# Optimization experiments

Hardware: AMD Instinct MI355X
Metric: run time of the kernel (lower is better)

## Reference

```python
import jax, jax.numpy as jnp
import numpy as np

D = 128        # feature dim (hard-coded 128 split in source)
C = 16         # number of classes
N_S = 1600     # support set size (C * 100 shots)
Q = 32768      # number of query samples
HID = 128      # Class_Adap hidden width


def _class_centers(support_feat_inv, support_features, support_labels):
    # per-class mean of both support tensors (ComputeClassCenters)
    ones = jnp.ones((support_labels.shape[0],), support_feat_inv.dtype)
    counts = jax.ops.segment_sum(ones, support_labels, num_segments=C)
    counts = jnp.maximum(counts, 1.0)[:, None]                     # [C,1]
    mean_s = jax.ops.segment_sum(support_feat_inv, support_labels, num_segments=C) / counts   # [C,D]
    pre_s = jax.ops.segment_sum(support_features, support_labels, num_segments=C) / counts    # [C,D]
    return mean_s, pre_s


def setup_inputs() -> dict:
    key = jax.random.key(0)
    ks = jax.random.split(key, 6)
    return {
        "support_feat_inv": jax.random.normal(ks[0], (N_S, D), jnp.float32),
        "support_features": jax.random.normal(ks[1], (N_S, D), jnp.float32),
        "query_features": jax.random.normal(ks[2], (Q, D), jnp.float32),
        "W1": jax.random.normal(ks[3], (2 * D + 1, HID), jnp.float32) * 0.05,
        "b1": jnp.zeros((HID,), jnp.float32),
        "W2": jax.random.normal(ks[4], (HID, 1), jnp.float32) * 0.05,
        "b2": jnp.zeros((1,), jnp.float32),
        "support_labels": jax.random.randint(ks[5], (N_S,), 0, C),
        "query_labels": jax.random.randint(jax.random.fold_in(key, 7), (Q,), 0, C),
    }


def reference(support_feat_inv, support_features, query_features, W1, b1, W2, b2,
              support_labels, query_labels) -> jnp.ndarray:
    mean_s, pre_s = _class_centers(support_feat_inv, support_features, support_labels)
    q = query_features[:, None, :]                                  # [Q,1,D]
    gated = jax.nn.sigmoid(mean_s)[None, :, :] * q                  # [Q,C,D]
    q_full = jnp.broadcast_to(q, gated.shape)                       # [Q,C,D]
    inp = jnp.concatenate([q_full, gated], axis=-1)                 # [Q,C,2D]
    # AdaptiveAvgPool2d((None, D)) on [C,1,2D]: average adjacent pairs along last dim
    pooled = inp.reshape(Q, C, D, 2).mean(axis=-1)                  # [Q,C,D]
    # inner/outer product: sum(pre_support * query) per class
    outer = jnp.sum(pre_s[None, :, :] * q, axis=-1, keepdims=True)  # [Q,C,1]
    ext = jnp.concatenate([inp, outer], axis=-1)                    # [Q,C,2D+1]
    # Class_Adap tiny MLP -> per-class scalar weight
    h = jax.nn.relu(jnp.einsum('qce,eh->qch', ext, W1) + b1)        # [Q,C,HID]
    w = jax.nn.sigmoid(jnp.einsum('qch,ho->qco', h, W2) + b2)       # [Q,C,1]
    agg = jnp.sum(pooled * w, axis=1)                               # [Q,D]
    return agg + query_features                                     # residual (query_feature[0])
```

## Files before the change

kernel.cpp:

```cpp
#include <hip/hip_runtime.h>
#include <hip/hip_bf16.h>
#include <stdint.h>

#define DD 128
#define CC 16
#define NS 1600
#define QQ 32768
#define NBLK 64
#define PLW 65

typedef __attribute__((ext_vector_type(8))) short short8;
typedef __attribute__((ext_vector_type(4))) short short4v;
typedef __attribute__((ext_vector_type(4))) float f32x4;

__device__ inline short f2bf(float x) {
  union { float f; uint32_t u; } v; v.f = x;
  uint32_t r = (v.u + 0x7FFFu + ((v.u >> 16) & 1u)) >> 16;
  return (short)r;
}

__device__ inline uint32_t pk2bf(float lo, float hi) {
  __hip_bfloat162 h = __float22bfloat162_rn(make_float2(lo, hi));
  union { __hip_bfloat162 h2; uint32_t u; } v; v.h2 = h;
  return v.u;
}

__device__ inline float bfbits2f(uint32_t hi16bits) {
  union { uint32_t u; float f; } v; v.u = hi16bits;
  return v.f;
}

__global__ __launch_bounds__(256) void prep_kernel(
    const float* __restrict__ sfi, const float* __restrict__ sf,
    const int* __restrict__ labels, const float* __restrict__ qf,
    float* __restrict__ partA, float* __restrict__ partB,
    float* __restrict__ pcnt, short* __restrict__ qbf) {
  const int t = threadIdx.x;

  if (blockIdx.x >= NBLK) {
    const size_t cb = (size_t)(blockIdx.x - NBLK) * (128 * DD);
#pragma unroll
    for (int i = 0; i < 16; ++i) {
      const size_t off = cb + ((size_t)i * 256 + t) * 4;
      f32x4 f = *(const f32x4*)(qf + off);
      union { short4v s; uint32_t u[2]; } r;
      r.u[0] = pk2bf(f[0], f[1]);
      r.u[1] = pk2bf(f[2], f[3]);
      *(short4v*)(qbf + off) = r.s;
    }
    return;
  }

  __shared__ float accA[2][CC][DD];
  __shared__ float accB[2][CC][DD];
  __shared__ float cnt[2][CC];
  const int d = t & 127, s = t >> 7;
  for (int i = t; i < 2 * CC * DD; i += 256) {
    ((float*)accA)[i] = 0.f;
    ((float*)accB)[i] = 0.f;
  }
  if (t < 2 * CC) ((float*)cnt)[t] = 0.f;
  __syncthreads();

  const int base = blockIdx.x * (NS / NBLK);
  for (int i = s; i < NS / NBLK; i += 2) {
    const int r = base + i;
    const int lbl = labels[r];
    accA[s][lbl][d] += sfi[(size_t)r * DD + d];
    accB[s][lbl][d] += sf[(size_t)r * DD + d];
    if (d == 0) cnt[s][lbl] += 1.f;
  }
  __syncthreads();

  float* pa = partA + (size_t)blockIdx.x * (CC * DD);
  float* pb = partB + (size_t)blockIdx.x * (CC * DD);
  for (int i = t; i < CC * DD; i += 256) {
    pa[i] = ((float*)accA)[i] + ((float*)accA)[CC * DD + i];
    pb[i] = ((float*)accB)[i] + ((float*)accB)[CC * DD + i];
  }
  if (t < CC) pcnt[blockIdx.x * CC + t] = cnt[0][t] + cnt[1][t];
}

__global__ __launch_bounds__(256) void build_wt_kernel(
    const float* __restrict__ W1, const float* __restrict__ partA,
    const float* __restrict__ partB, const float* __restrict__ pcnt,
    float* __restrict__ sg_out, short* __restrict__ WtTg) {
  __shared__ float sgc[DD], prc[DD];
  const int c = blockIdx.x, t = threadIdx.x;

  float cnt = 0.f;
  for (int b = 0; b < NBLK; ++b) cnt += pcnt[b * CC + c];
  cnt = fmaxf(cnt, 1.f);
  if (t < 128) {
    float a = 0.f;
    for (int b = 0; b < NBLK; ++b) a += partA[(size_t)b * (CC * DD) + c * DD + t];
    const float m = a / cnt;
    const float s = 1.f / (1.f + expf(-m));
    sgc[t] = s;
    sg_out[c * DD + t] = s;
  } else {
    const int d = t - 128;
    float a = 0.f;
    for (int b = 0; b < NBLK; ++b) a += partB[(size_t)b * (CC * DD) + c * DD + d];
    prc[d] = a / cnt;
  }
  __syncthreads();

  for (int it = 0; it < 8; ++it) {
    const int u = it * 256 + t;
    const int w_ = u >> 8;
    const int kb = (u >> 6) & 3;
    const int lane = u & 63;
    const int j = w_ * 16 + (lane & 15);
    const int e0 = kb * 32 + (lane >> 4) * 8;
    short8 r;
#pragma unroll
    for (int rr = 0; rr < 8; ++rr) {
      const int e = e0 + rr;
      float v = W1[e * DD + j] + sgc[e] * W1[(DD + e) * DD + j] +
                prc[e] * W1[2 * DD * DD + j];
      r[rr] = f2bf(v);
    }
    *(short8*)(WtTg + ((size_t)c * 2048 + u) * 8) = r;
  }
}

__global__ __launch_bounds__(512, 4) void main_kernel(
    const short* __restrict__ qbf, const short* __restrict__ WtTg,
    const float* __restrict__ b1, const float* __restrict__ W2,
    const float* __restrict__ b2, const float* __restrict__ sg,
    float* __restrict__ out) {
  __shared__ float p_pln[4 * 64 * PLW];
  __shared__ float w_lds[64][17];

  const int tid = threadIdx.x;
  const int lane = tid & 63;
  const int w = tid >> 6;
  const int l15 = lane & 15, l4 = lane >> 4;
  const int qbase = blockIdx.x * 64;

  short8 bq[4][4];
#pragma unroll
  for (int qn = 0; qn < 4; ++qn) {
    const short* qrow = qbf + (size_t)(qbase + qn * 16 + l15) * DD;
#pragma unroll
    for (int kb = 0; kb < 4; ++kb)
      bq[qn][kb] = *(const short8*)(qrow + kb * 32 + l4 * 8);
  }

  const f32x4 b1v = *(const f32x4*)(b1 + w * 16 + l4 * 4);
  const f32x4 w2v = *(const f32x4*)(W2 + w * 16 + l4 * 4);
  const float b2s = b2[0];

  const char* wbase = (const char*)WtTg + w * 4096 + lane * 16;

#define LOADW(dst, cls)                                                     \
  {                                                                         \
    _Pragma("unroll") for (int kb = 0; kb < 4; ++kb) dst[kb] =              \
        *(const short8*)(wbase + (size_t)(cls)*32768 + kb * 1024);          \
  }

#define COMPUTE(wf, cls)                                                    \
  {                                                                         \
    const int slot = (((cls)&7) * 8 + w) * PLW + lane;                      \
    _Pragma("unroll") for (int qp = 0; qp < 2; ++qp) {                      \
      f32x4 a0 = b1v, a1 = b1v;                                             \
      _Pragma("unroll") for (int kb = 0; kb < 4; ++kb) {                    \
        a0 = __builtin_amdgcn_mfma_f32_16x16x32_bf16(wf[kb],                \
                                                     bq[2 * qp][kb], a0,    \
                                                     0, 0, 0);              \
        a1 = __builtin_amdgcn_mfma_f32_16x16x32_bf16(wf[kb],                \
                                                     bq[2 * qp + 1][kb],    \
                                                     a1, 0, 0, 0);          \
      }                                                                     \
      float p0 = 0.f, p1 = 0.f;                                             \
      _Pragma("unroll") for (int i = 0; i < 4; ++i) {                       \
        p0 += fmaxf(a0[i], 0.f) * w2v[i];                                   \
        p1 += fmaxf(a1[i], 0.f) * w2v[i];                                   \
      }                                                                     \
      p_pln[(2 * qp) * (64 * PLW) + slot] = p0;                             \
      p_pln[(2 * qp + 1) * (64 * PLW) + slot] = p1;                         \
    }                                                                       \
  }

#define REDUCE(hf)                                                          \
  {                                                                         \
    __syncthreads();                                                        \
    if (tid < 256) {                                                        \
      const int qp = tid >> 7, c7 = (tid >> 4) & 7, lr = tid & 15;          \
      _Pragma("unroll") for (int qq = 0; qq < 2; ++qq) {                    \
        const int qn = qp * 2 + qq;                                         \
        const float* pb = p_pln + qn * (64 * PLW) + c7 * (8 * PLW) + lr;    \
        float sacc = 0.f;                                                   \
        _Pragma("unroll") for (int wv = 0; wv < 8; ++wv)                    \
            _Pragma("unroll") for (int g = 0; g < 4; ++g) sacc +=           \
            pb[wv * PLW + g * 16];                                          \
        w_lds[qn * 16 + lr][(hf)*8 + c7] =                                  \
            1.f / (1.f + __expf(-(sacc + b2s)));                            \
      }                                                                     \
    }                                                                       \
    __syncthreads();                                                        \
  }

  short8 wfA[4], wfB[4];
  LOADW(wfA, 0);
  for (int cp = 0; cp < CC; cp += 2) {
    LOADW(wfB, cp + 1);
    COMPUTE(wfA, cp);
    if (cp + 2 < CC) LOADW(wfA, cp + 2);
    COMPUTE(wfB, cp + 1);
    if (cp == 6) REDUCE(0);
    if (cp == 14) REDUCE(1);
  }
#undef LOADW
#undef COMPUTE
#undef REDUCE

  {
    float2 sgv[16];
#pragma unroll
    for (int c = 0; c < 16; ++c)
      sgv[c] = *(const float2*)(sg + c * DD + 2 * lane);

#pragma unroll
    for (int qi = 0; qi < 8; ++qi) {
      const int ql = qi * 8 + w;
      const int q = qbase + ql;
      float Sv = 0.f, swx = 0.f, swy = 0.f;
#pragma unroll
      for (int c = 0; c < 16; ++c) {
        const float wc = w_lds[ql][c];
        Sv += wc;
        swx += wc * sgv[c].x;
        swy += wc * sgv[c].y;
      }
      const uint16_t* row = (const uint16_t*)(qbf + (size_t)q * DD);
      const uint32_t pair = *(const uint32_t*)(row + 2 * lane);
      const float q0 = bfbits2f(pair << 16);
      const float q1 = bfbits2f(pair & 0xFFFF0000u);
      const float qlo = bfbits2f((uint32_t)row[lane] << 16);
      const float qhi = bfbits2f((uint32_t)row[64 + lane] << 16);

      float* orow = out + (size_t)q * DD;
      orow[lane] = 0.5f * (q0 + q1) * Sv + qlo;
      orow[64 + lane] = 0.5f * (q0 * swx + q1 * swy) + qhi;
    }
  }
}

extern "C" void kernel_launch(void* const* d_in, const int* in_sizes, int n_in,
                              void* d_out, int out_size, void* d_ws, size_t ws_size,
                              hipStream_t stream) {
  const float* sfi = (const float*)d_in[0];
  const float* sf  = (const float*)d_in[1];
  const float* qf  = (const float*)d_in[2];
  const float* W1  = (const float*)d_in[3];
  const float* b1  = (const float*)d_in[4];
  const float* W2  = (const float*)d_in[5];
  const float* b2  = (const float*)d_in[6];
  const int* slab  = (const int*)d_in[7];
  float* out = (float*)d_out;

  float* sg    = (float*)d_ws;
  short* WtTg  = (short*)(sg + CC * DD);
  float* partA = (float*)(WtTg + CC * DD * DD);
  float* partB = partA + NBLK * CC * DD;
  float* pcnt  = partB + NBLK * CC * DD;
  short* qbf   = (short*)(pcnt + NBLK * CC);

  prep_kernel<<<NBLK + QQ / 128, 256, 0, stream>>>(sfi, sf, slab, qf, partA,
                                                   partB, pcnt, qbf);
  build_wt_kernel<<<CC, 256, 0, stream>>>(W1, partA, partB, pcnt, sg, WtTg);
  main_kernel<<<QQ / 64, 512, 0, stream>>>(qbf, WtTg, b1, W2, b2, sg, out);
}
```

Measured before the change: 53.91 us.

## Stage per-class W tiles in LDS via async global_load_lds with double buffering

```diff
diff --git a/kernel.cpp b/kernel.cpp
--- a/kernel.cpp
+++ b/kernel.cpp
@@ -7,7 +7,7 @@
 #define NS 1600
 #define QQ 32768
 #define NBLK 64
-#define PLW 65
+#define QT 128
 
 typedef __attribute__((ext_vector_type(8))) short short8;
 typedef __attribute__((ext_vector_type(4))) short short4v;
@@ -107,12 +107,10 @@
   __syncthreads();
 
   for (int it = 0; it < 8; ++it) {
-    const int u = it * 256 + t;
-    const int w_ = u >> 8;
-    const int kb = (u >> 6) & 3;
-    const int lane = u & 63;
-    const int j = w_ * 16 + (lane & 15);
-    const int e0 = kb * 32 + (lane >> 4) * 8;
+    const int p = it * 256 + t;
+    const int j = it * 16 + (t >> 4);
+    const int eb = (t & 15) ^ ((t >> 4) & 7);
+    const int e0 = eb * 8;
     short8 r;
 #pragma unroll
     for (int rr = 0; rr < 8; ++rr) {
@@ -121,100 +119,125 @@
                 prc[e] * W1[2 * DD * DD + j];
       r[rr] = f2bf(v);
     }
-    *(short8*)(WtTg + ((size_t)c * 2048 + u) * 8) = r;
-  }
-}
-
-__global__ __launch_bounds__(512, 4) void main_kernel(
+    *(short8*)(WtTg + ((size_t)c * 2048 + p) * 8) = r;
+  }
+}
+
+__global__ __launch_bounds__(1024, 4) void main_kernel(
     const short* __restrict__ qbf, const short* __restrict__ WtTg,
     const float* __restrict__ b1, const float* __restrict__ W2,
     const float* __restrict__ b2, const float* __restrict__ sg,
     float* __restrict__ out) {
-  __shared__ float p_pln[4 * 64 * PLW];
-  __shared__ float w_lds[64][17];
+  __shared__ __align__(16) char Wl[2][32768];
+  __shared__ float p_pln[2][16][65][4];
+  __shared__ float w_lds[QT][17];
+  __shared__ float b1_l[DD], w2_l[DD];
 
   const int tid = threadIdx.x;
   const int lane = tid & 63;
   const int w = tid >> 6;
+  const int wq = w >> 3;
+  const int wj = w & 7;
   const int l15 = lane & 15, l4 = lane >> 4;
-  const int qbase = blockIdx.x * 64;
+  const int qbase = blockIdx.x * QT;
+
+  if (tid < DD) { b1_l[tid] = b1[tid]; w2_l[tid] = W2[tid]; }
+  const float b2s = b2[0];
+
+  const char* gsrc = (const char*)WtTg;
+#pragma unroll
+  for (int i = 0; i < 2; ++i) {
+    const int off = i * 16384 + tid * 16;
+    __builtin_amdgcn_global_load_lds(
+        (const __attribute__((address_space(1))) uint32_t*)(gsrc + off),
+        (__attribute__((address_space(3))) uint32_t*)(&Wl[0][0] + off), 16, 0, 0);
+  }
 
   short8 bq[4][4];
 #pragma unroll
   for (int qn = 0; qn < 4; ++qn) {
-    const short* qrow = qbf + (size_t)(qbase + qn * 16 + l15) * DD;
+    const short* qrow = qbf + (size_t)(qbase + wq * 64 + qn * 16 + l15) * DD;
 #pragma unroll
     for (int kb = 0; kb < 4; ++kb)
       bq[qn][kb] = *(const short8*)(qrow + kb * 32 + l4 * 8);
   }
 
-  const f32x4 b1v = *(const f32x4*)(b1 + w * 16 + l4 * 4);
-  const f32x4 w2v = *(const f32x4*)(W2 + w * 16 + l4 * 4);
-  const float b2s = b2[0];
-
-  const char* wbase = (const char*)WtTg + w * 4096 + lane * 16;
-
-#define LOADW(dst, cls)                                                     \
-  {                                                                         \
-    _Pragma("unroll") for (int kb = 0; kb < 4; ++kb) dst[kb] =              \
-        *(const short8*)(wbase + (size_t)(cls)*32768 + kb * 1024);          \
-  }
-
-#define COMPUTE(wf, cls)                                                    \
-  {                                                                         \
-    const int slot = (((cls)&7) * 8 + w) * PLW + lane;                      \
-    _Pragma("unroll") for (int qp = 0; qp < 2; ++qp) {                      \
-      f32x4 a0 = b1v, a1 = b1v;                                             \
-      _Pragma("unroll") for (int kb = 0; kb < 4; ++kb) {                    \
-        a0 = __builtin_amdgcn_mfma_f32_16x16x32_bf16(wf[kb],                \
-                                                     bq[2 * qp][kb], a0,    \
-                                                     0, 0, 0);              \
-        a1 = __builtin_amdgcn_mfma_f32_16x16x32_bf16(wf[kb],                \
-                                                     bq[2 * qp + 1][kb],    \
-                                                     a1, 0, 0, 0);          \
-      }                                                                     \
-      float p0 = 0.f, p1 = 0.f;                                             \
-      _Pragma("unroll") for (int i = 0; i < 4; ++i) {                       \
-        p0 += fmaxf(a0[i], 0.f) * w2v[i];                                   \
-        p1 += fmaxf(a1[i], 0.f) * w2v[i];                                   \
-      }                                                                     \
-      p_pln[(2 * qp) * (64 * PLW) + slot] = p0;                             \
-      p_pln[(2 * qp + 1) * (64 * PLW) + slot] = p1;                         \
-    }                                                                       \
-  }
-
-#define REDUCE(hf)                                                          \
-  {                                                                         \
-    __syncthreads();                                                        \
-    if (tid < 256) {                                                        \
-      const int qp = tid >> 7, c7 = (tid >> 4) & 7, lr = tid & 15;          \
-      _Pragma("unroll") for (int qq = 0; qq < 2; ++qq) {                    \
-        const int qn = qp * 2 + qq;                                         \
-        const float* pb = p_pln + qn * (64 * PLW) + c7 * (8 * PLW) + lr;    \
-        float sacc = 0.f;                                                   \
-        _Pragma("unroll") for (int wv = 0; wv < 8; ++wv)                    \
-            _Pragma("unroll") for (int g = 0; g < 4; ++g) sacc +=           \
-            pb[wv * PLW + g * 16];                                          \
-        w_lds[qn * 16 + lr][(hf)*8 + c7] =                                  \
-            1.f / (1.f + __expf(-(sacc + b2s)));                            \
-      }                                                                     \
-    }                                                                       \
-    __syncthreads();                                                        \
-  }
-
-  short8 wfA[4], wfB[4];
-  LOADW(wfA, 0);
-  for (int cp = 0; cp < CC; cp += 2) {
-    LOADW(wfB, cp + 1);
-    COMPUTE(wfA, cp);
-    if (cp + 2 < CC) LOADW(wfA, cp + 2);
-    COMPUTE(wfB, cp + 1);
-    if (cp == 6) REDUCE(0);
-    if (cp == 14) REDUCE(1);
-  }
-#undef LOADW
-#undef COMPUTE
-#undef REDUCE
+  int aoff[4];
+#pragma unroll
+  for (int kb = 0; kb < 4; ++kb)
+    aoff[kb] = (wj * 16 + l15) * 256 + (((kb * 4 + l4) ^ (l15 & 7)) << 4);
+
+  const f32x4* b1p = (const f32x4*)(b1_l + wj * 16 + l4 * 4);
+  const f32x4* w2p = (const f32x4*)(w2_l + wj * 16 + l4 * 4);
+
+  asm volatile("s_waitcnt vmcnt(0)" ::: "memory");
+  __syncthreads();
+
+  for (int c = 0; c < CC; ++c) {
+    const int buf = c & 1;
+    if (c + 1 < CC) {
+      const char* gc = gsrc + (size_t)(c + 1) * 32768;
+#pragma unroll
+      for (int i = 0; i < 2; ++i) {
+        const int off = i * 16384 + tid * 16;
+        __builtin_amdgcn_global_load_lds(
+            (const __attribute__((address_space(1))) uint32_t*)(gc + off),
+            (__attribute__((address_space(3))) uint32_t*)(&Wl[buf ^ 1][0] + off),
+            16, 0, 0);
+      }
+    }
+
+    {
+      const char* wb = &Wl[buf][0];
+      short8 A[4];
+#pragma unroll
+      for (int kb = 0; kb < 4; ++kb) A[kb] = *(const short8*)(wb + aoff[kb]);
+      const f32x4 b1v = *b1p;
+      const f32x4 w2v = *w2p;
+      f32x4 pv;
+#pragma unroll
+      for (int qp = 0; qp < 2; ++qp) {
+        f32x4 a0 = {0.f, 0.f, 0.f, 0.f}, a1 = {0.f, 0.f, 0.f, 0.f};
+#pragma unroll
+        for (int kb = 0; kb < 4; ++kb) {
+          a0 = __builtin_amdgcn_mfma_f32_16x16x32_bf16(A[kb], bq[2 * qp][kb],
+                                                       a0, 0, 0, 0);
+          a1 = __builtin_amdgcn_mfma_f32_16x16x32_bf16(A[kb], bq[2 * qp + 1][kb],
+                                                       a1, 0, 0, 0);
+        }
+        float p0 = 0.f, p1 = 0.f;
+#pragma unroll
+        for (int i = 0; i < 4; ++i) {
+          p0 += fmaxf(a0[i] + b1v[i], 0.f) * w2v[i];
+          p1 += fmaxf(a1[i] + b1v[i], 0.f) * w2v[i];
+        }
+        pv[2 * qp] = p0;
+        pv[2 * qp + 1] = p1;
+      }
+      *(f32x4*)&p_pln[buf][w][lane][0] = pv;
+    }
+
+    asm volatile("s_waitcnt vmcnt(0)" ::: "memory");
+    __syncthreads();
+
+    if (c & 1) {
+      if (tid < 256) {
+        const int c1 = tid >> 7;
+        const int ql = tid & 127;
+        const int rq = ql >> 6;
+        const int qn = (ql >> 4) & 3;
+        const int rl = ql & 15;
+        float s = 0.f;
+#pragma unroll
+        for (int j8 = 0; j8 < 8; ++j8)
+#pragma unroll
+          for (int g = 0; g < 4; ++g)
+            s += p_pln[c1][rq * 8 + j8][g * 16 + rl][qn];
+        w_lds[ql][(c - 1) + c1] = 1.f / (1.f + __expf(-(s + b2s)));
+      }
+      __syncthreads();
+    }
+  }
 
   {
     float2 sgv[16];
@@ -224,7 +247,7 @@
 
 #pragma unroll
     for (int qi = 0; qi < 8; ++qi) {
-      const int ql = qi * 8 + w;
+      const int ql = qi * 16 + w;
       const int q = qbase + ql;
       float Sv = 0.f, swx = 0.f, swy = 0.f;
 #pragma unroll
@@ -271,5 +294,5 @@
   prep_kernel<<<NBLK + QQ / 128, 256, 0, stream>>>(sfi, sf, slab, qf, partA,
                                                    partB, pcnt, qbf);
   build_wt_kernel<<<CC, 256, 0, stream>>>(W1, partA, partB, pcnt, sg, WtTg);
-  main_kernel<<<QQ / 64, 512, 0, stream>>>(qbf, WtTg, b1, W2, b2, sg, out);
-}
+  main_kernel<<<QQ / QT, 1024, 0, stream>>>(qbf, WtTg, b1, W2, b2, sg, out);
+}
```

Result: slower. 71.08 us (+31.8%).

## Fuse query bf16 conversion into main kernel and drop prep pass

Applied to the files above, without the earlier changes.

```diff
diff --git a/kernel.cpp b/kernel.cpp
--- a/kernel.cpp
+++ b/kernel.cpp
@@ -10,7 +10,6 @@
 #define PLW 65
 
 typedef __attribute__((ext_vector_type(8))) short short8;
-typedef __attribute__((ext_vector_type(4))) short short4v;
 typedef __attribute__((ext_vector_type(4))) float f32x4;
 
 __device__ inline short f2bf(float x) {
@@ -25,35 +24,14 @@
   return v.u;
 }
 
-__device__ inline float bfbits2f(uint32_t hi16bits) {
-  union { uint32_t u; float f; } v; v.u = hi16bits;
-  return v.f;
-}
-
-__global__ __launch_bounds__(256) void prep_kernel(
+__global__ __launch_bounds__(256) void centers_partial(
     const float* __restrict__ sfi, const float* __restrict__ sf,
-    const int* __restrict__ labels, const float* __restrict__ qf,
-    float* __restrict__ partA, float* __restrict__ partB,
-    float* __restrict__ pcnt, short* __restrict__ qbf) {
-  const int t = threadIdx.x;
-
-  if (blockIdx.x >= NBLK) {
-    const size_t cb = (size_t)(blockIdx.x - NBLK) * (128 * DD);
-#pragma unroll
-    for (int i = 0; i < 16; ++i) {
-      const size_t off = cb + ((size_t)i * 256 + t) * 4;
-      f32x4 f = *(const f32x4*)(qf + off);
-      union { short4v s; uint32_t u[2]; } r;
-      r.u[0] = pk2bf(f[0], f[1]);
-      r.u[1] = pk2bf(f[2], f[3]);
-      *(short4v*)(qbf + off) = r.s;
-    }
-    return;
-  }
-
+    const int* __restrict__ labels, float* __restrict__ partA,
+    float* __restrict__ partB, float* __restrict__ pcnt) {
   __shared__ float accA[2][CC][DD];
   __shared__ float accB[2][CC][DD];
   __shared__ float cnt[2][CC];
+  const int t = threadIdx.x;
   const int d = t & 127, s = t >> 7;
   for (int i = t; i < 2 * CC * DD; i += 256) {
     ((float*)accA)[i] = 0.f;
@@ -125,8 +103,8 @@
   }
 }
 
-__global__ __launch_bounds__(512, 4) void main_kernel(
-    const short* __restrict__ qbf, const short* __restrict__ WtTg,
+__global__ __launch_bounds__(512, 2) void main_kernel(
+    const float* __restrict__ qf, const short* __restrict__ WtTg,
     const float* __restrict__ b1, const float* __restrict__ W2,
     const float* __restrict__ b2, const float* __restrict__ sg,
     float* __restrict__ out) {
@@ -142,10 +120,19 @@
   short8 bq[4][4];
 #pragma unroll
   for (int qn = 0; qn < 4; ++qn) {
-    const short* qrow = qbf + (size_t)(qbase + qn * 16 + l15) * DD;
-#pragma unroll
-    for (int kb = 0; kb < 4; ++kb)
-      bq[qn][kb] = *(const short8*)(qrow + kb * 32 + l4 * 8);
+    const float* qrow = qf + (size_t)(qbase + qn * 16 + l15) * DD;
+#pragma unroll
+    for (int kb = 0; kb < 4; ++kb) {
+      const float* p0 = qrow + kb * 32 + l4 * 8;
+      f32x4 f0 = *(const f32x4*)(p0);
+      f32x4 f1 = *(const f32x4*)(p0 + 4);
+      union { short8 s; uint32_t u[4]; } r;
+      r.u[0] = pk2bf(f0[0], f0[1]);
+      r.u[1] = pk2bf(f0[2], f0[3]);
+      r.u[2] = pk2bf(f1[0], f1[1]);
+      r.u[3] = pk2bf(f1[2], f1[3]);
+      bq[qn][kb] = r.s;
+    }
   }
 
   const f32x4 b1v = *(const f32x4*)(b1 + w * 16 + l4 * 4);
@@ -234,16 +221,14 @@
         swx += wc * sgv[c].x;
         swy += wc * sgv[c].y;
       }
-      const uint16_t* row = (const uint16_t*)(qbf + (size_t)q * DD);
-      const uint32_t pair = *(const uint32_t*)(row + 2 * lane);
-      const float q0 = bfbits2f(pair << 16);
-      const float q1 = bfbits2f(pair & 0xFFFF0000u);
-      const float qlo = bfbits2f((uint32_t)row[lane] << 16);
-      const float qhi = bfbits2f((uint32_t)row[64 + lane] << 16);
+      const float* qrow = qf + (size_t)q * DD;
+      const float2 qp2 = *(const float2*)(qrow + 2 * lane);
+      const float qlo = qrow[lane];
+      const float qhi = qrow[64 + lane];
 
       float* orow = out + (size_t)q * DD;
-      orow[lane] = 0.5f * (q0 + q1) * Sv + qlo;
-      orow[64 + lane] = 0.5f * (q0 * swx + q1 * swy) + qhi;
+      orow[lane] = 0.5f * (qp2.x + qp2.y) * Sv + qlo;
+      orow[64 + lane] = 0.5f * (qp2.x * swx + qp2.y * swy) + qhi;
     }
   }
 }
@@ -266,10 +251,8 @@
   float* partA = (float*)(WtTg + CC * DD * DD);
   float* partB = partA + NBLK * CC * DD;
   float* pcnt  = partB + NBLK * CC * DD;
-  short* qbf   = (short*)(pcnt + NBLK * CC);
-
-  prep_kernel<<<NBLK + QQ / 128, 256, 0, stream>>>(sfi, sf, slab, qf, partA,
-                                                   partB, pcnt, qbf);
+
+  centers_partial<<<NBLK, 256, 0, stream>>>(sfi, sf, slab, partA, partB, pcnt);
   build_wt_kernel<<<CC, 256, 0, stream>>>(W1, partA, partB, pcnt, sg, WtTg);
-  main_kernel<<<QQ / 64, 512, 0, stream>>>(qbf, WtTg, b1, W2, b2, sg, out);
-}
+  main_kernel<<<QQ / 64, 512, 0, stream>>>(qf, WtTg, b1, W2, b2, sg, out);
+}
```

New measurement: 62.59 us. 1.16x slower.

## Reduce hidden partials with wave shuffles, shrink LDS staging, fully unroll class loop

Applied to the files above, without the earlier changes.

```diff
diff --git a/kernel.cpp b/kernel.cpp
--- a/kernel.cpp
+++ b/kernel.cpp
@@ -7,7 +7,6 @@
 #define NS 1600
 #define QQ 32768
 #define NBLK 64
-#define PLW 65
 
 typedef __attribute__((ext_vector_type(8))) short short8;
 typedef __attribute__((ext_vector_type(4))) short short4v;
@@ -125,12 +124,12 @@
   }
 }
 
-__global__ __launch_bounds__(512, 4) void main_kernel(
+__global__ __launch_bounds__(512, 2) void main_kernel(
     const short* __restrict__ qbf, const short* __restrict__ WtTg,
     const float* __restrict__ b1, const float* __restrict__ W2,
     const float* __restrict__ b2, const float* __restrict__ sg,
     float* __restrict__ out) {
-  __shared__ float p_pln[4 * 64 * PLW];
+  __shared__ float p_pln[8][8][64];
   __shared__ float w_lds[64][17];
 
   const int tid = threadIdx.x;
@@ -162,7 +161,7 @@
 
 #define COMPUTE(wf, cls)                                                    \
   {                                                                         \
-    const int slot = (((cls)&7) * 8 + w) * PLW + lane;                      \
+    float pv[4];                                                            \
     _Pragma("unroll") for (int qp = 0; qp < 2; ++qp) {                      \
       f32x4 a0 = b1v, a1 = b1v;                                             \
       _Pragma("unroll") for (int kb = 0; kb < 4; ++kb) {                    \
@@ -178,40 +177,52 @@
         p0 += fmaxf(a0[i], 0.f) * w2v[i];                                   \
         p1 += fmaxf(a1[i], 0.f) * w2v[i];                                   \
       }                                                                     \
-      p_pln[(2 * qp) * (64 * PLW) + slot] = p0;                             \
-      p_pln[(2 * qp + 1) * (64 * PLW) + slot] = p1;                         \
+      pv[2 * qp] = p0;                                                      \
+      pv[2 * qp + 1] = p1;                                                  \
+    }                                                                       \
+    _Pragma("unroll") for (int qn = 0; qn < 4; ++qn) {                      \
+      pv[qn] += __shfl_xor(pv[qn], 16);                                     \
+      pv[qn] += __shfl_xor(pv[qn], 32);                                     \
+    }                                                                       \
+    if (l4 == 0) {                                                          \
+      _Pragma("unroll") for (int qn = 0; qn < 4; ++qn)                      \
+          p_pln[(cls)&7][w][qn * 16 + l15] = pv[qn];                        \
     }                                                                       \
   }
 
 #define REDUCE(hf)                                                          \
   {                                                                         \
     __syncthreads();                                                        \
-    if (tid < 256) {                                                        \
-      const int qp = tid >> 7, c7 = (tid >> 4) & 7, lr = tid & 15;          \
-      _Pragma("unroll") for (int qq = 0; qq < 2; ++qq) {                    \
-        const int qn = qp * 2 + qq;                                         \
-        const float* pb = p_pln + qn * (64 * PLW) + c7 * (8 * PLW) + lr;    \
-        float sacc = 0.f;                                                   \
-        _Pragma("unroll") for (int wv = 0; wv < 8; ++wv)                    \
-            _Pragma("unroll") for (int g = 0; g < 4; ++g) sacc +=           \
-            pb[wv * PLW + g * 16];                                          \
-        w_lds[qn * 16 + lr][(hf)*8 + c7] =                                  \
-            1.f / (1.f + __expf(-(sacc + b2s)));                            \
-      }                                                                     \
+    {                                                                       \
+      const int rc = tid >> 6, rq = tid & 63;                               \
+      float s = 0.f;                                                        \
+      _Pragma("unroll") for (int wv = 0; wv < 8; ++wv)                      \
+          s += p_pln[rc][wv][rq];                                           \
+      w_lds[rq][(hf)*8 + rc] = 1.f / (1.f + __expf(-(s + b2s)));            \
     }                                                                       \
     __syncthreads();                                                        \
   }
 
   short8 wfA[4], wfB[4];
   LOADW(wfA, 0);
-  for (int cp = 0; cp < CC; cp += 2) {
-    LOADW(wfB, cp + 1);
-    COMPUTE(wfA, cp);
-    if (cp + 2 < CC) LOADW(wfA, cp + 2);
-    COMPUTE(wfB, cp + 1);
-    if (cp == 6) REDUCE(0);
-    if (cp == 14) REDUCE(1);
-  }
+  LOADW(wfB, 1);  COMPUTE(wfA, 0);
+  LOADW(wfA, 2);  COMPUTE(wfB, 1);
+  LOADW(wfB, 3);  COMPUTE(wfA, 2);
+  LOADW(wfA, 4);  COMPUTE(wfB, 3);
+  LOADW(wfB, 5);  COMPUTE(wfA, 4);
+  LOADW(wfA, 6);  COMPUTE(wfB, 5);
+  LOADW(wfB, 7);  COMPUTE(wfA, 6);
+  LOADW(wfA, 8);  COMPUTE(wfB, 7);
+  REDUCE(0);
+  LOADW(wfB, 9);  COMPUTE(wfA, 8);
+  LOADW(wfA, 10); COMPUTE(wfB, 9);
+  LOADW(wfB, 11); COMPUTE(wfA, 10);
+  LOADW(wfA, 12); COMPUTE(wfB, 11);
+  LOADW(wfB, 13); COMPUTE(wfA, 12);
+  LOADW(wfA, 14); COMPUTE(wfB, 13);
+  LOADW(wfB, 15); COMPUTE(wfA, 14);
+  COMPUTE(wfB, 15);
+  REDUCE(1);
 #undef LOADW
 #undef COMPUTE
 #undef REDUCE
```

Result: no change. 54.67 us (+1.4%).
